# Performance work log

Measured on AMD Instinct MI355X. Metric: run time of the kernel, lower is better.

## Reference

```python
import jax, jax.numpy as jnp
import numpy as np

ELEM, EMBD = 512, 512

def setup_inputs() -> dict:
    key = jax.random.key(0)
    ks = jax.random.split(key, 7)
    s = 1.0 / np.sqrt(ELEM)
    return {
        "x": jax.random.normal(ks[0], (8, 2048, ELEM), dtype=jnp.float32),
        "Wq": jax.random.normal(ks[1], (ELEM, EMBD), dtype=jnp.float32) * s,
        "bq": jnp.zeros((EMBD,), dtype=jnp.float32),
        "Wk": jax.random.normal(ks[2], (ELEM, EMBD), dtype=jnp.float32) * s,
        "bk": jnp.zeros((EMBD,), dtype=jnp.float32),
        "Wv": jax.random.normal(ks[3], (ELEM, EMBD), dtype=jnp.float32) * s,
        "bv": jnp.zeros((EMBD,), dtype=jnp.float32),
    }

def reference(x, Wq, bq, Wk, bk, Wv, bv):
    # x: [N, S, E]
    q = x @ Wq + bq            # [N, S, D]
    k = x @ Wk + bk            # [N, S, D]
    v = x @ Wv + bv            # [N, S, D]
    # NOTE: original has no 1/sqrt(d) scaling.
    logits = jnp.einsum('nsd,ntd->nst', q, k)   # [N, S, S]
    attn = jax.nn.softmax(logits, axis=-1)
    return jnp.einsum('nst,ntd->nsd', attn, v)  # [N, S, D]
```

## Files before the change

### kernel.cpp

```cpp
#include <hip/hip_runtime.h>
#include <hip/hip_fp16.h>

#define SEQ 2048
#define DIM 512

typedef __attribute__((ext_vector_type(8))) short short8;
typedef __attribute__((ext_vector_type(4))) float f32x4;
typedef _Float16 h8 __attribute__((ext_vector_type(8)));
typedef _Float16 h4 __attribute__((ext_vector_type(4)));

#define MFMA16(a, b, c) __builtin_amdgcn_mfma_f32_16x16x32_f16((a), (b), (c), 0, 0, 0)

#define GLOAD_LDS16(g, l)                                                              \
    __builtin_amdgcn_global_load_lds(                                                  \
        (const __attribute__((address_space(1))) unsigned int*)(g),                    \
        (__attribute__((address_space(3))) unsigned int*)(l), 16, 0, 0)

template <int MODE>
__device__ __forceinline__ void gemmw_body(
    int L, char* sm,
    const _Float16* __restrict__ A, const _Float16* __restrict__ B,
    const float* __restrict__ biasA, const float* __restrict__ biasB,
    _Float16* __restrict__ o0, _Float16* __restrict__ ovt,
    float* __restrict__ ofp, int bat0) {
    constexpr int T  = (MODE == 0) ? 16 : (MODE == 1) ? 8 : 32;
    constexpr int PA = (MODE == 2) ? 4096 : 512;
    constexpr int PB = (MODE == 0) ? 1024 : (MODE == 1) ? 512 : 2048;

    int tid = threadIdx.x, wid = tid >> 6, lane = tid & 63, r = lane & 15, g = lane >> 4;
    int wm = wid >> 1, wn = wid & 1;
    int xcd = L & 7, s = L >> 3;
    int m0, n0, bz = 0;
    if (MODE == 0)      { m0 = (xcd * 8 + (s >> 2)) * 256; n0 = (s & 3) * 128; }
    else if (MODE == 1) { m0 = (xcd * 8 + (s >> 3)) * 256; n0 = (s & 7) * 128; }
    else                { m0 = xcd * 256; bz = s >> 2; n0 = (s & 3) * 128; }

    const _Float16 *Ab, *Bb;
    if (MODE == 2) {
        int b = bat0 + bz;
        Ab = A + (size_t)bz * (SEQ * 4096) + (size_t)m0 * 4096;
        Bb = B + (size_t)b * (512 * SEQ) + (size_t)n0 * 2048;
    } else {
        Ab = A + (size_t)m0 * 512;
        Bb = B + (size_t)n0 * PB;
    }

    const char* gA[4];
    const char* gB[2];
    int ldsA[4], ldsB[2];
#pragma unroll
    for (int j = 0; j < 4; ++j) {
        int ci = j * 512 + tid;
        int row = ci >> 3, cl = ci & 7;
        int col16 = cl ^ (row & 7);
        gA[j] = (const char*)Ab + (size_t)row * (PA * 2) + col16 * 16;
        ldsA[j] = ci * 16;
    }
#pragma unroll
    for (int j = 0; j < 2; ++j) {
        int ci = j * 512 + tid;
        int row = ci >> 3, cl = ci & 7;
        int col16 = cl ^ (row & 7);
        gB[j] = (const char*)Bb + (size_t)row * (PB * 2) + col16 * 16;
        ldsB[j] = ci * 16;
    }
    int offA[4][2], offB[4][2];
#pragma unroll
    for (int m = 0; m < 4; ++m) {
        int rowA = wm * 64 + m * 16 + r;
        int rowB = wn * 64 + m * 16 + r;
#pragma unroll
        for (int ks = 0; ks < 2; ++ks) {
            offA[m][ks] = rowA * 128 + (((ks * 4 + g) ^ (rowA & 7)) * 16);
            offB[m][ks] = rowB * 128 + (((ks * 4 + g) ^ (rowB & 7)) * 16);
        }
    }

    f32x4 acc[4][4];
#pragma unroll
    for (int m = 0; m < 4; ++m)
#pragma unroll
        for (int n = 0; n < 4; ++n) acc[m][n] = (f32x4)(0.0f);

    auto STG = [&](int t, int b) {
        int ka = (MODE == 0) ? ((t & 7) * 128) : (t * 128);
        int kb = t * 128;
        char* dA = sm + b * 49152;
        char* dB = sm + b * 49152 + 32768;
#pragma unroll
        for (int j = 0; j < 4; ++j) GLOAD_LDS16(gA[j] + ka, dA + ldsA[j]);
#pragma unroll
        for (int j = 0; j < 2; ++j) GLOAD_LDS16(gB[j] + kb, dB + ldsB[j]);
    };

    STG(0, 0);
    STG(1, 1);
    asm volatile("s_waitcnt vmcnt(6)" ::: "memory");
    __builtin_amdgcn_s_barrier();

#pragma unroll
    for (int t = 0; t < T; ++t) {
        const int buf = t % 3;
        if (t + 2 < T) STG(t + 2, (t + 2) % 3);
        const char* bA = sm + buf * 49152;
        const char* bB = sm + buf * 49152 + 32768;
        h8 af[4][2], bf[4][2];
#pragma unroll
        for (int m = 0; m < 4; ++m)
#pragma unroll
            for (int ks = 0; ks < 2; ++ks) {
                af[m][ks] = *(const h8*)(bA + offA[m][ks]);
                bf[m][ks] = *(const h8*)(bB + offB[m][ks]);
            }
        __builtin_amdgcn_s_setprio(1);
#pragma unroll
        for (int ks = 0; ks < 2; ++ks)
#pragma unroll
            for (int m = 0; m < 4; ++m)
#pragma unroll
                for (int n = 0; n < 4; ++n)
                    acc[m][n] = MFMA16(af[m][ks], bf[n][ks], acc[m][n]);
        __builtin_amdgcn_s_setprio(0);
        if (t + 2 < T) asm volatile("s_waitcnt vmcnt(6)" ::: "memory");
        else if (t + 1 < T) asm volatile("s_waitcnt vmcnt(0)" ::: "memory");
        if (t + 1 < T) __builtin_amdgcn_s_barrier();
    }

    if (MODE == 0) {
#pragma unroll
        for (int n = 0; n < 4; ++n) {
            int col = n0 + wn * 64 + n * 16 + r;
            float bi = biasA[col];
#pragma unroll
            for (int m = 0; m < 4; ++m) {
                int grow0 = m0 + wm * 64 + m * 16 + 4 * g;
                for (int reg = 0; reg < 4; ++reg)
                    o0[(size_t)(grow0 + reg) * 512 + col] =
                        (_Float16)(acc[m][n][reg] + bi);
            }
        }
    } else if (MODE == 1) {
        int p = n0 >> 9, ncl = n0 & 511;
        if (p == 0) {
#pragma unroll
            for (int n = 0; n < 4; ++n) {
                int col = ncl + wn * 64 + n * 16 + r;
                float bi = biasA[col];
#pragma unroll
                for (int m = 0; m < 4; ++m) {
                    int grow0 = m0 + wm * 64 + m * 16 + 4 * g;
                    for (int reg = 0; reg < 4; ++reg)
                        o0[(size_t)(grow0 + reg) * 512 + col] =
                            (_Float16)(acc[m][n][reg] + bi);
                }
            }
        } else {
            __syncthreads();
            _Float16* tt = (_Float16*)sm;
#pragma unroll
            for (int n = 0; n < 4; ++n) {
                int dloc = wn * 64 + n * 16 + r;
                float bi = biasB[ncl + dloc];
#pragma unroll
                for (int m = 0; m < 4; ++m) {
                    int sloc = wm * 64 + m * 16 + 4 * g;
                    h4 pv;
                    pv[0] = (_Float16)(acc[m][n][0] + bi);
                    pv[1] = (_Float16)(acc[m][n][1] + bi);
                    pv[2] = (_Float16)(acc[m][n][2] + bi);
                    pv[3] = (_Float16)(acc[m][n][3] + bi);
                    *(h4*)(&tt[dloc * 264 + sloc]) = pv;
                }
            }
            __syncthreads();
            int b = m0 >> 11, s0b = m0 & 2047;
            int drow = tid >> 2, part = tid & 3;
            const char* src = (const char*)(tt + drow * 264 + part * 64);
            char* dst = (char*)(ovt + (size_t)b * (512 * 2048) +
                                (size_t)(ncl + drow) * 2048 + s0b + part * 64);
#pragma unroll
            for (int j = 0; j < 8; ++j)
                *(short8*)(dst + j * 16) = *(const short8*)(src + j * 16);
        }
    } else {
        int b = bat0 + bz;
#pragma unroll
        for (int n = 0; n < 4; ++n) {
            int col = n0 + wn * 64 + n * 16 + r;
#pragma unroll
            for (int m = 0; m < 4; ++m) {
                int grow0 = m0 + wm * 64 + m * 16 + 4 * g;
                for (int reg = 0; reg < 4; ++reg)
                    ofp[(size_t)(b * SEQ + grow0 + reg) * 512 + col] = acc[m][n][reg];
            }
        }
    }
}

__global__ __launch_bounds__(512, 1) void gemmw_proj(
    const _Float16* __restrict__ xh,
    const _Float16* __restrict__ wq, const _Float16* __restrict__ wkv,
    const float* __restrict__ bq, const float* __restrict__ bk,
    const float* __restrict__ bv,
    _Float16* __restrict__ qh, _Float16* __restrict__ kh,
    _Float16* __restrict__ vt) {
    extern __shared__ char sm[];
    int L = blockIdx.x;
    if (L < 256)
        gemmw_body<0>(L, sm, xh, wq, bq, nullptr, qh, nullptr, nullptr, 0);
    else
        gemmw_body<1>(L - 256, sm, xh, wkv, bk, bv, kh, vt, nullptr, 0);
}

__global__ __launch_bounds__(512, 1) void gemmw_pv(
    const _Float16* __restrict__ pbuf, const _Float16* __restrict__ vt,
    float* __restrict__ out, int bat0) {
    extern __shared__ char sm[];
    gemmw_body<2>(blockIdx.x, sm, pbuf, vt, nullptr, nullptr, nullptr, nullptr,
                  out, bat0);
}

__global__ __launch_bounds__(256) void gemmn_qk(
    const _Float16* __restrict__ A, const _Float16* __restrict__ B,
    float* __restrict__ of, int bat0) {
    __shared__ char sm[2 * 32768];
    constexpr int T = 8, PA = 512, PB = 512;

    int tid = threadIdx.x, wid = tid >> 6, lane = tid & 63, r = lane & 15, g = lane >> 4;
    int mw = wid >> 1, nw = wid & 1;
    int L = blockIdx.x, xcd = L & 7, s = L >> 3;
    int bz = s >> 5;
    int rem = s & 31;
    int m0 = (xcd * 2 + (rem >> 4)) * 128;
    int n0 = (rem & 15) * 128;

    int b = bat0 + bz;
    const _Float16* Ab = A + ((size_t)(b * SEQ) + m0) * 512;
    const _Float16* Bb = B + ((size_t)(b * SEQ) + n0) * 512;

    const char* gA[4];
    const char* gB[4];
    int ldsw[4];
#pragma unroll
    for (int j = 0; j < 4; ++j) {
        int ci = (j * 4 + wid) * 64 + lane;
        int row = ci >> 3, cl = ci & 7;
        int col16 = cl ^ (row & 7);
        gA[j] = (const char*)Ab + (size_t)row * (PA * 2) + col16 * 16;
        gB[j] = (const char*)Bb + (size_t)row * (PB * 2) + col16 * 16;
        ldsw[j] = (j * 4 + wid) * 1024;
    }
    int offA[4][2], offB[4][2];
#pragma unroll
    for (int m = 0; m < 4; ++m) {
        int rowA = mw * 64 + m * 16 + r;
        int rowB = nw * 64 + m * 16 + r;
#pragma unroll
        for (int ks = 0; ks < 2; ++ks) {
            offA[m][ks] = rowA * 128 + (((ks * 4 + g) ^ (rowA & 7)) * 16);
            offB[m][ks] = rowB * 128 + (((ks * 4 + g) ^ (rowB & 7)) * 16);
        }
    }

    f32x4 acc[4][4];
#pragma unroll
    for (int m = 0; m < 4; ++m)
#pragma unroll
        for (int n = 0; n < 4; ++n) acc[m][n] = (f32x4)(0.0f);

    auto STG = [&](int t, int bb) {
        int ka = t * 128, kb = t * 128;
        char* dA = sm + bb * 32768;
        char* dB = sm + bb * 32768 + 16384;
#pragma unroll
        for (int j = 0; j < 4; ++j) {
            GLOAD_LDS16(gA[j] + ka, dA + ldsw[j]);
            GLOAD_LDS16(gB[j] + kb, dB + ldsw[j]);
        }
    };

    STG(0, 0);
    asm volatile("s_waitcnt vmcnt(0)" ::: "memory");
    __builtin_amdgcn_s_barrier();

#pragma unroll
    for (int t = 0; t < T; ++t) {
        const int buf = t & 1;
        if (t + 1 < T) STG(t + 1, buf ^ 1);
        const char* bA = sm + buf * 32768;
        const char* bB = sm + buf * 32768 + 16384;
        h8 af[4][2], bf[4][2];
#pragma unroll
        for (int m = 0; m < 4; ++m)
#pragma unroll
            for (int ks = 0; ks < 2; ++ks) {
                af[m][ks] = *(const h8*)(bA + offA[m][ks]);
                bf[m][ks] = *(const h8*)(bB + offB[m][ks]);
            }
#pragma unroll
        for (int ks = 0; ks < 2; ++ks)
#pragma unroll
            for (int m = 0; m < 4; ++m)
#pragma unroll
                for (int n = 0; n < 4; ++n)
                    acc[m][n] = MFMA16(af[m][ks], bf[n][ks], acc[m][n]);
        if (t + 1 < T) {
            asm volatile("s_waitcnt vmcnt(0)" ::: "memory");
            __builtin_amdgcn_s_barrier();
        }
    }

    float* sb = of + (size_t)bz * (SEQ * (size_t)SEQ);
#pragma unroll
    for (int n = 0; n < 4; ++n) {
        int col = n0 + nw * 64 + n * 16 + r;
#pragma unroll
        for (int m = 0; m < 4; ++m) {
            int grow0 = m0 + mw * 64 + m * 16 + 4 * g;
            for (int reg = 0; reg < 4; ++reg)
                sb[(size_t)(grow0 + reg) * SEQ + col] = acc[m][n][reg];
        }
    }
}

__global__ __launch_bounds__(256) void k3_softmax(float* __restrict__ sbuf) {
    size_t row = blockIdx.x;
    float* srow = sbuf + row * SEQ;
    int tid = threadIdx.x, lane = tid & 63, wid = tid >> 6;
    float4 v0 = *(const float4*)(srow + tid * 8);
    float4 v1 = *(const float4*)(srow + tid * 8 + 4);
    float m = fmaxf(fmaxf(fmaxf(v0.x, v0.y), fmaxf(v0.z, v0.w)),
                    fmaxf(fmaxf(v1.x, v1.y), fmaxf(v1.z, v1.w)));
    for (int d = 1; d < 64; d <<= 1) m = fmaxf(m, __shfl_xor(m, d));
    __shared__ float red1[4], red2[4];
    if (lane == 0) red1[wid] = m;
    __syncthreads();
    m = fmaxf(fmaxf(red1[0], red1[1]), fmaxf(red1[2], red1[3]));
    float e[8];
    e[0] = __expf(v0.x - m); e[1] = __expf(v0.y - m);
    e[2] = __expf(v0.z - m); e[3] = __expf(v0.w - m);
    e[4] = __expf(v1.x - m); e[5] = __expf(v1.y - m);
    e[6] = __expf(v1.z - m); e[7] = __expf(v1.w - m);
    float s = ((e[0] + e[1]) + (e[2] + e[3])) + ((e[4] + e[5]) + (e[6] + e[7]));
    for (int d = 1; d < 64; d <<= 1) s += __shfl_xor(s, d);
    if (lane == 0) red2[wid] = s;
    __syncthreads();
    s = (red2[0] + red2[1]) + (red2[2] + red2[3]);
    float inv = 1.0f / s;
    h8 ph;
    for (int j = 0; j < 8; ++j) ph[j] = (_Float16)(e[j] * inv);
    *(h8*)((char*)srow + (size_t)tid * 16) = ph;
}

__global__ __launch_bounds__(256) void k0_prep(
    const float* __restrict__ x,
    const float* __restrict__ Wq, const float* __restrict__ Wk,
    const float* __restrict__ Wv,
    _Float16* __restrict__ wq, _Float16* __restrict__ wkv,
    _Float16* __restrict__ xh) {
    int blk = blockIdx.x;
    if (blk < 3072) {
        int idx = blk * 256 + threadIdx.x;
        int p = idx >> 18;
        int rem = idx & 262143;
        int k = rem >> 9, n = rem & 511;
        if (p == 0) {
            float w = Wq[rem];
            _Float16 h = (_Float16)w;
            wq[(size_t)n * 1024 + k] = h;
            wq[(size_t)n * 1024 + 512 + k] = (_Float16)(w - (float)h);
        } else if (p == 1) {
            wkv[(size_t)n * 512 + k] = (_Float16)Wk[rem];
        } else {
            wkv[(size_t)(512 + n) * 512 + k] = (_Float16)Wv[rem];
        }
    } else {
        size_t i = (size_t)((blk - 3072) * 256 + threadIdx.x) * 4;
        float4 v = *(const float4*)(x + i);
        h4 h;
        h[0] = (_Float16)v.x; h[1] = (_Float16)v.y;
        h[2] = (_Float16)v.z; h[3] = (_Float16)v.w;
        *(h4*)(xh + i) = h;
    }
}

extern "C" void kernel_launch(void* const* d_in, const int* in_sizes, int n_in,
                              void* d_out, int out_size, void* d_ws, size_t ws_size,
                              hipStream_t stream) {
    const float* x  = (const float*)d_in[0];
    const float* Wq = (const float*)d_in[1];
    const float* bq = (const float*)d_in[2];
    const float* Wk = (const float*)d_in[3];
    const float* bk = (const float*)d_in[4];
    const float* Wv = (const float*)d_in[5];
    const float* bv = (const float*)d_in[6];
    float* out = (float*)d_out;

    char* ws = (char*)d_ws;
    const size_t QSZ = 16777216;
    _Float16* wq  = (_Float16*)(ws);
    _Float16* wkv = (_Float16*)(ws + 1048576);
    _Float16* xh = (_Float16*)(ws + 3145728);
    _Float16* qh = (_Float16*)(ws + 3145728 + 1 * QSZ);
    _Float16* kh = (_Float16*)(ws + 3145728 + 2 * QSZ);
    _Float16* vt = (_Float16*)(ws + 3145728 + 3 * QSZ);
    const size_t sbase = 3145728 + 4 * QSZ;

    const int LDSW = 3 * 49152;
    hipFuncSetAttribute((const void*)gemmw_proj,
                        hipFuncAttributeMaxDynamicSharedMemorySize, LDSW);
    hipFuncSetAttribute((const void*)gemmw_pv,
                        hipFuncAttributeMaxDynamicSharedMemorySize, LDSW);

    k0_prep<<<11264, 256, 0, stream>>>(x, Wq, Wk, Wv, wq, wkv, xh);
    gemmw_proj<<<768, 512, LDSW, stream>>>(xh, wq, wkv, bq, bk, bv, qh, kh, vt);

    size_t avail = (ws_size > sbase) ? (ws_size - sbase) : 0;
    int chunk = (int)(avail / QSZ);
    if (chunk < 1) chunk = 1;
    if (chunk > 8) chunk = 8;
    float* sc = (float*)(ws + sbase);
    for (int b0 = 0; b0 < 8; b0 += chunk) {
        int nb = (8 - b0 < chunk) ? (8 - b0) : chunk;
        gemmn_qk<<<nb * 256, 256, 0, stream>>>(qh, kh, sc, b0);
        k3_softmax<<<dim3(nb * SEQ), 256, 0, stream>>>(sc);
        gemmw_pv<<<nb * 32, 512, LDSW, stream>>>((const _Float16*)sc, vt, out, b0);
    }
}
```

Before: 169.8 us.

## Rewrite QK^T GEMM as 256x256-tile 8-wave kernel with staged LDS pipeline

Replaces the 128x128, 4-wave QK score GEMM with a 256x256 tile kernel using 8 waves and 128KB dynamic LDS. Each K-step is split into four quadrant phases, with global->LDS loads for future tiles interleaved between MFMA clusters. The phases are bracketed by barriers and raise wave priority during the MFMA blocks. The aim is better operand reuse per tile and overlap of memory loads with compute. The cost is fewer blocks (64 per batch), more barriers per iteration and one block per CU occupancy.

New measurement: 172.8 us. No clear change (+1.8%).

```diff
diff --git a/kernel.cpp b/kernel.cpp
--- a/kernel.cpp
+++ b/kernel.cpp
@@ -15,6 +15,13 @@
     __builtin_amdgcn_global_load_lds(                                                  \
         (const __attribute__((address_space(1))) unsigned int*)(g),                    \
         (__attribute__((address_space(3))) unsigned int*)(l), 16, 0, 0)
+
+#define BAR() __builtin_amdgcn_s_barrier()
+#define WAITL()                                                                        \
+    do {                                                                               \
+        asm volatile("s_waitcnt lgkmcnt(0)" ::: "memory");                             \
+        __builtin_amdgcn_sched_barrier(0);                                             \
+    } while (0)
 
 template <int MODE>
 __device__ __forceinline__ void gemmw_body(
@@ -220,105 +227,161 @@
                   out, bat0);
 }
 
-__global__ __launch_bounds__(256) void gemmn_qk(
+__global__ __launch_bounds__(512, 1) void gemm8_qk(
     const _Float16* __restrict__ A, const _Float16* __restrict__ B,
     float* __restrict__ of, int bat0) {
-    __shared__ char sm[2 * 32768];
-    constexpr int T = 8, PA = 512, PB = 512;
+    extern __shared__ char sm[];
+    constexpr int T = 8;
 
     int tid = threadIdx.x, wid = tid >> 6, lane = tid & 63, r = lane & 15, g = lane >> 4;
-    int mw = wid >> 1, nw = wid & 1;
+    int wm = wid >> 2, wn = wid & 3;
     int L = blockIdx.x, xcd = L & 7, s = L >> 3;
-    int bz = s >> 5;
-    int rem = s & 31;
-    int m0 = (xcd * 2 + (rem >> 4)) * 128;
-    int n0 = (rem & 15) * 128;
-
+    int m0 = xcd * 256, bz = s >> 3, n0 = (s & 7) * 256;
     int b = bat0 + bz;
-    const _Float16* Ab = A + ((size_t)(b * SEQ) + m0) * 512;
-    const _Float16* Bb = B + ((size_t)(b * SEQ) + n0) * 512;
-
-    const char* gA[4];
-    const char* gB[4];
-    int ldsw[4];
-#pragma unroll
-    for (int j = 0; j < 4; ++j) {
-        int ci = (j * 4 + wid) * 64 + lane;
-        int row = ci >> 3, cl = ci & 7;
-        int col16 = cl ^ (row & 7);
-        gA[j] = (const char*)Ab + (size_t)row * (PA * 2) + col16 * 16;
-        gB[j] = (const char*)Bb + (size_t)row * (PB * 2) + col16 * 16;
-        ldsw[j] = (j * 4 + wid) * 1024;
-    }
-    int offA[4][2], offB[4][2];
-#pragma unroll
-    for (int m = 0; m < 4; ++m) {
-        int rowA = mw * 64 + m * 16 + r;
-        int rowB = nw * 64 + m * 16 + r;
-#pragma unroll
-        for (int ks = 0; ks < 2; ++ks) {
-            offA[m][ks] = rowA * 128 + (((ks * 4 + g) ^ (rowA & 7)) * 16);
-            offB[m][ks] = rowB * 128 + (((ks * 4 + g) ^ (rowB & 7)) * 16);
-        }
-    }
-
-    f32x4 acc[4][4];
-#pragma unroll
-    for (int m = 0; m < 4; ++m)
+    const char* Ag = (const char*)(A + ((size_t)(b * SEQ) + m0) * 512);
+    const char* Bg = (const char*)(B + ((size_t)(b * SEQ) + n0) * 512);
+
+    const char* sA[2];
+    const char* sB[2];
+    int dci[2];
+#pragma unroll
+    for (int j = 0; j < 2; ++j) {
+        int ci = j * 512 + tid;
+        int rl = ci >> 3, cl = ci & 7;
+        size_t so = (size_t)rl * 1024 + (size_t)((cl ^ (rl & 7)) * 16);
+        sA[j] = Ag + so;
+        sB[j] = Bg + so;
+        dci[j] = ci * 16;
+    }
+    auto STG = [&](int op, int t, int h) {
+        const char* s0 = op ? sB[0] : sA[0];
+        const char* s1 = op ? sB[1] : sA[1];
+        char* dst = sm + (op ? 65536 : 0) + (t & 1) * 32768 + h * 16384;
+        size_t hof = (size_t)h * 131072 + (size_t)t * 128;
+        GLOAD_LDS16(s0 + hof, dst + dci[0]);
+        GLOAD_LDS16(s1 + hof, dst + dci[1]);
+    };
+
+    int offA[4][2], offB[2][2];
+#pragma unroll
+    for (int mf = 0; mf < 4; ++mf) {
+        int row = wm * 128 + mf * 16 + r;
+#pragma unroll
+        for (int ks = 0; ks < 2; ++ks)
+            offA[mf][ks] = row * 128 + (((ks * 4 + g) ^ (row & 7)) * 16);
+    }
+#pragma unroll
+    for (int nf = 0; nf < 2; ++nf) {
+        int row = wn * 64 + nf * 16 + r;
+#pragma unroll
+        for (int ks = 0; ks < 2; ++ks)
+            offB[nf][ks] = row * 128 + (((ks * 4 + g) ^ (row & 7)) * 16);
+    }
+
+    f32x4 acc[8][4];
+#pragma unroll
+    for (int m = 0; m < 8; ++m)
 #pragma unroll
         for (int n = 0; n < 4; ++n) acc[m][n] = (f32x4)(0.0f);
 
-    auto STG = [&](int t, int bb) {
-        int ka = t * 128, kb = t * 128;
-        char* dA = sm + bb * 32768;
-        char* dB = sm + bb * 32768 + 16384;
-#pragma unroll
-        for (int j = 0; j < 4; ++j) {
-            GLOAD_LDS16(gA[j] + ka, dA + ldsw[j]);
-            GLOAD_LDS16(gB[j] + kb, dB + ldsw[j]);
-        }
-    };
-
-    STG(0, 0);
-    asm volatile("s_waitcnt vmcnt(0)" ::: "memory");
-    __builtin_amdgcn_s_barrier();
-
+#pragma unroll
+    for (int tt = 0; tt < 2; ++tt) {
+        STG(0, tt, 0); STG(0, tt, 1); STG(1, tt, 0); STG(1, tt, 1);
+    }
+    asm volatile("s_waitcnt vmcnt(8)" ::: "memory");
+    BAR();
+
+    h8 afq[4][2], bf0[2][2], bf1[2][2];
 #pragma unroll
     for (int t = 0; t < T; ++t) {
-        const int buf = t & 1;
-        if (t + 1 < T) STG(t + 1, buf ^ 1);
-        const char* bA = sm + buf * 32768;
-        const char* bB = sm + buf * 32768 + 16384;
-        h8 af[4][2], bf[4][2];
-#pragma unroll
-        for (int m = 0; m < 4; ++m)
-#pragma unroll
-            for (int ks = 0; ks < 2; ++ks) {
-                af[m][ks] = *(const h8*)(bA + offA[m][ks]);
-                bf[m][ks] = *(const h8*)(bB + offB[m][ks]);
-            }
-#pragma unroll
-        for (int ks = 0; ks < 2; ++ks)
-#pragma unroll
-            for (int m = 0; m < 4; ++m)
-#pragma unroll
-                for (int n = 0; n < 4; ++n)
-                    acc[m][n] = MFMA16(af[m][ks], bf[n][ks], acc[m][n]);
-        if (t + 1 < T) {
-            asm volatile("s_waitcnt vmcnt(0)" ::: "memory");
-            __builtin_amdgcn_s_barrier();
-        }
+        const char* bA = sm + (t & 1) * 32768;
+        const char* bB = sm + 65536 + (t & 1) * 32768;
+#pragma unroll
+        for (int mf = 0; mf < 4; ++mf)
+#pragma unroll
+            for (int ks = 0; ks < 2; ++ks)
+                afq[mf][ks] = *(const h8*)(bA + offA[mf][ks]);
+#pragma unroll
+        for (int nf = 0; nf < 2; ++nf)
+#pragma unroll
+            for (int ks = 0; ks < 2; ++ks)
+                bf0[nf][ks] = *(const h8*)(bB + offB[nf][ks]);
+        if (t >= 1 && t + 1 < T) STG(0, t + 1, 0);
+        BAR();
+        WAITL();
+        __builtin_amdgcn_s_setprio(1);
+#pragma unroll
+        for (int ks = 0; ks < 2; ++ks)
+#pragma unroll
+            for (int mf = 0; mf < 4; ++mf)
+#pragma unroll
+                for (int nf = 0; nf < 2; ++nf)
+                    acc[mf][nf] = MFMA16(afq[mf][ks], bf0[nf][ks], acc[mf][nf]);
+        __builtin_amdgcn_s_setprio(0);
+        BAR();
+#pragma unroll
+        for (int nf = 0; nf < 2; ++nf)
+#pragma unroll
+            for (int ks = 0; ks < 2; ++ks)
+                bf1[nf][ks] = *(const h8*)(bB + offB[nf][ks] + 4096);
+        if (t >= 1 && t + 1 < T) STG(0, t + 1, 1);
+        BAR();
+        WAITL();
+        __builtin_amdgcn_s_setprio(1);
+#pragma unroll
+        for (int ks = 0; ks < 2; ++ks)
+#pragma unroll
+            for (int mf = 0; mf < 4; ++mf)
+#pragma unroll
+                for (int nf = 0; nf < 2; ++nf)
+                    acc[mf][2 + nf] = MFMA16(afq[mf][ks], bf1[nf][ks], acc[mf][2 + nf]);
+        __builtin_amdgcn_s_setprio(0);
+        BAR();
+#pragma unroll
+        for (int mf = 0; mf < 4; ++mf)
+#pragma unroll
+            for (int ks = 0; ks < 2; ++ks)
+                afq[mf][ks] = *(const h8*)(bA + offA[mf][ks] + 8192);
+        if (t + 2 < T) STG(1, t + 2, 0);
+        BAR();
+        WAITL();
+        __builtin_amdgcn_s_setprio(1);
+#pragma unroll
+        for (int ks = 0; ks < 2; ++ks)
+#pragma unroll
+            for (int mf = 0; mf < 4; ++mf)
+#pragma unroll
+                for (int nf = 0; nf < 2; ++nf)
+                    acc[4 + mf][2 + nf] =
+                        MFMA16(afq[mf][ks], bf1[nf][ks], acc[4 + mf][2 + nf]);
+        __builtin_amdgcn_s_setprio(0);
+        BAR();
+        if (t + 2 < T) STG(1, t + 2, 1);
+        BAR();
+        WAITL();
+        __builtin_amdgcn_s_setprio(1);
+#pragma unroll
+        for (int ks = 0; ks < 2; ++ks)
+#pragma unroll
+            for (int mf = 0; mf < 4; ++mf)
+#pragma unroll
+                for (int nf = 0; nf < 2; ++nf)
+                    acc[4 + mf][nf] = MFMA16(afq[mf][ks], bf0[nf][ks], acc[4 + mf][nf]);
+        __builtin_amdgcn_s_setprio(0);
+        if (t < T - 2) asm volatile("s_waitcnt vmcnt(4)" ::: "memory");
+        else asm volatile("s_waitcnt vmcnt(0)" ::: "memory");
+        if (t + 1 < T) BAR();
     }
 
     float* sb = of + (size_t)bz * (SEQ * (size_t)SEQ);
 #pragma unroll
-    for (int n = 0; n < 4; ++n) {
-        int col = n0 + nw * 64 + n * 16 + r;
-#pragma unroll
-        for (int m = 0; m < 4; ++m) {
-            int grow0 = m0 + mw * 64 + m * 16 + 4 * g;
+    for (int nf = 0; nf < 4; ++nf) {
+        int col = n0 + wn * 64 + nf * 16 + r;
+#pragma unroll
+        for (int mf = 0; mf < 8; ++mf) {
+            int grow0 = m0 + wm * 128 + mf * 16 + 4 * g;
             for (int reg = 0; reg < 4; ++reg)
-                sb[(size_t)(grow0 + reg) * SEQ + col] = acc[m][n][reg];
+                sb[(size_t)(grow0 + reg) * SEQ + col] = acc[mf][nf][reg];
         }
     }
 }
@@ -407,10 +470,13 @@
     const size_t sbase = 3145728 + 4 * QSZ;
 
     const int LDSW = 3 * 49152;
+    const int LDS8 = 131072;
     hipFuncSetAttribute((const void*)gemmw_proj,
                         hipFuncAttributeMaxDynamicSharedMemorySize, LDSW);
     hipFuncSetAttribute((const void*)gemmw_pv,
                         hipFuncAttributeMaxDynamicSharedMemorySize, LDSW);
+    hipFuncSetAttribute((const void*)gemm8_qk,
+                        hipFuncAttributeMaxDynamicSharedMemorySize, LDS8);
 
     k0_prep<<<11264, 256, 0, stream>>>(x, Wq, Wk, Wv, wq, wkv, xh);
     gemmw_proj<<<768, 512, LDSW, stream>>>(xh, wq, wkv, bq, bk, bv, qh, kh, vt);
@@ -422,7 +488,7 @@
     float* sc = (float*)(ws + sbase);
     for (int b0 = 0; b0 < 8; b0 += chunk) {
         int nb = (8 - b0 < chunk) ? (8 - b0) : chunk;
-        gemmn_qk<<<nb * 256, 256, 0, stream>>>(qh, kh, sc, b0);
+        gemm8_qk<<<nb * 64, 512, LDS8, stream>>>(qh, kh, sc, b0);
         k3_softmax<<<dim3(nb * SEQ), 256, 0, stream>>>(sc);
         gemmw_pv<<<nb * 32, 512, LDSW, stream>>>((const _Float16*)sc, vt, out, b0);
     }
```
